# Performance work log

Hardware: AMD Instinct MI355X
Metric: run time of the kernel (lower is better)

The kernel has to match this reference:

```python
import jax, jax.numpy as jnp
import numpy as np

B, L, D_MODEL, H, D_QKV = 4, 2048, 1024, 16, 64
SCALE = float(D_MODEL) ** 0.5  # note: source scales by sqrt(d_model), not sqrt(d_qkv)


def setup_inputs() -> dict:
    key = jax.random.key(0)
    ks = jax.random.split(key, 6)
    xavier_qkv = (2.0 / (D_MODEL + D_QKV)) ** 0.5
    xavier_fc = (2.0 / (H * D_QKV + D_MODEL)) ** 0.5
    return {
        "x": jax.random.normal(ks[0], (B, L, D_MODEL), dtype=jnp.float32),
        "mask": jnp.ones((B, L), dtype=jnp.int32),
        "w_q": jax.random.normal(ks[1], (H, D_MODEL, D_QKV), dtype=jnp.float32) * xavier_qkv,
        "w_k": jax.random.normal(ks[2], (H, D_MODEL, D_QKV), dtype=jnp.float32) * xavier_qkv,
        "w_v": jax.random.normal(ks[3], (H, D_MODEL, D_QKV), dtype=jnp.float32) * xavier_qkv,
        "fc_w": jax.random.normal(ks[4], (D_MODEL, H * D_QKV), dtype=jnp.float32) * xavier_fc,
        "fc_b": jnp.zeros((D_MODEL,), dtype=jnp.float32),
    }


def reference(x, mask, w_q, w_k, w_v, fc_w, fc_b):
    # x: [B, L, M]; per-head projections via einsum, as in the source
    q = jnp.einsum('blm,hmd->blhd', x, w_q)
    k = jnp.einsum('blm,hmd->blhd', x, w_k)
    v = jnp.einsum('blm,hmd->blhd', x, w_v)
    scores = jnp.einsum('blhd,bkhd->bhlk', q, k)  # [B, H, L, L]
    m = mask[:, None, None, :]  # unsqueeze(1).unsqueeze(2)
    scores = jnp.where(m == 0, jnp.asarray(-1e9, scores.dtype), scores)
    logits = jax.nn.softmax(scores / SCALE, axis=3)
    # Faithful to source einsum 'bhlk,blhd->blhd' (k is summed out of logits only)
    out = jnp.einsum('bhlk,blhd->blhd', logits, v)
    out = out.reshape(x.shape[0], x.shape[1], H * D_QKV)
    return out @ fc_w.T + fc_b
```

## Files before the change

kernel.cpp:

```cpp
#include <hip/hip_runtime.h>
#include <hip/hip_bf16.h>


typedef __attribute__((ext_vector_type(8))) short bf16x8;
typedef __attribute__((ext_vector_type(4))) float f32x4;

__device__ __forceinline__ f32x4 mfma16(bf16x8 a, bf16x8 b, f32x4 c) {
  return __builtin_amdgcn_mfma_f32_16x16x32_bf16(a, b, c, 0, 0, 0);
}

__device__ __forceinline__ unsigned short f2b(float f) {
  unsigned int u = __builtin_bit_cast(unsigned int, f);
  return (unsigned short)((u + 0x7fffu + ((u >> 16) & 1u)) >> 16);
}

__device__ __forceinline__ bf16x8 cvt8(float4 a, float4 b) {
  bf16x8 r;
  r[0] = (short)f2b(a.x); r[1] = (short)f2b(a.y); r[2] = (short)f2b(a.z); r[3] = (short)f2b(a.w);
  r[4] = (short)f2b(b.x); r[5] = (short)f2b(b.y); r[6] = (short)f2b(b.z); r[7] = (short)f2b(b.w);
  return r;
}

__device__ __forceinline__ void gld_lds16(const void* g, void* l) {
  __builtin_amdgcn_global_load_lds((const __attribute__((address_space(1))) unsigned int*)g,
                                   (__attribute__((address_space(3))) unsigned int*)l, 16, 0, 0);
}

__global__ __launch_bounds__(256) void prep(const float* __restrict__ x,
                                            const float* __restrict__ wv,
                                            const float* __restrict__ fcw,
                                            unsigned short* __restrict__ xb,
                                            unsigned short* __restrict__ wcT) {
  int bid = blockIdx.x, t = threadIdx.x;
  int wid = t >> 6, lane = t & 63, l16 = lane & 15, quad = lane >> 4;

  if (bid < 256) {
    int wr = wid >> 1, wc = wid & 1;
    int row0 = (bid >> 4) * 64 + wr * 32;
    int col0 = (bid & 15) * 64 + wc * 32;
    f32x4 acc[2][2];
#pragma unroll
    for (int a = 0; a < 2; a++)
#pragma unroll
      for (int b = 0; b < 2; b++) acc[a][b] = (f32x4){0.f, 0.f, 0.f, 0.f};

    float4 A0[2][2], B0[2][2];
#define LOADK(kk, Ad, Bd)                                                            \
    {                                                                                \
      int h_ = (kk) >> 6, d_ = (kk) & 63;                                            \
      _Pragma("unroll")                                                              \
      for (int rt = 0; rt < 2; rt++) {                                               \
        const float* pa = fcw + (row0 + rt * 16 + l16) * 1024 + (kk);                \
        Ad[rt][0] = *reinterpret_cast<const float4*>(pa);                            \
        Ad[rt][1] = *reinterpret_cast<const float4*>(pa + 4);                        \
      }                                                                              \
      _Pragma("unroll")                                                              \
      for (int ct = 0; ct < 2; ct++) {                                               \
        const float* pb = wv + h_ * 65536 + (col0 + ct * 16 + l16) * 64 + d_;        \
        Bd[ct][0] = *reinterpret_cast<const float4*>(pb);                            \
        Bd[ct][1] = *reinterpret_cast<const float4*>(pb + 4);                        \
      }                                                                              \
    }
    LOADK(quad * 8, A0, B0);
    for (int k0 = 0; k0 < 1024; k0 += 32) {
      float4 A1[2][2], B1[2][2];
      if (k0 < 992) LOADK(k0 + 32 + quad * 8, A1, B1);
      bf16x8 af[2], bfr[2];
#pragma unroll
      for (int rt = 0; rt < 2; rt++) af[rt] = cvt8(A0[rt][0], A0[rt][1]);
#pragma unroll
      for (int ct = 0; ct < 2; ct++) bfr[ct] = cvt8(B0[ct][0], B0[ct][1]);
#pragma unroll
      for (int rt = 0; rt < 2; rt++)
#pragma unroll
        for (int ct = 0; ct < 2; ct++) acc[rt][ct] = mfma16(af[rt], bfr[ct], acc[rt][ct]);
#pragma unroll
      for (int a = 0; a < 2; a++)
#pragma unroll
        for (int b = 0; b < 2; b++) { A0[a][b] = A1[a][b]; B0[a][b] = B1[a][b]; }
    }
#undef LOADK
#pragma unroll
    for (int rt = 0; rt < 2; rt++)
#pragma unroll
      for (int ct = 0; ct < 2; ct++) {
        int j0 = row0 + rt * 16 + quad * 4;
        int m = col0 + ct * 16 + l16;
#pragma unroll
        for (int r = 0; r < 4; r++) wcT[(j0 + r) * 1024 + m] = f2b(acc[rt][ct][r]);
      }
  } else {
    int base0 = (bid - 256) << 15;
#pragma unroll
    for (int i = 0; i < 16; i++) {
      int idx = base0 + i * 2048 + t * 8;
      float4 a = *reinterpret_cast<const float4*>(x + idx);
      float4 b = *reinterpret_cast<const float4*>(x + idx + 4);
      *reinterpret_cast<bf16x8*>(xb + idx) = cvt8(a, b);
    }
  }
}

__global__ __launch_bounds__(256, 4) void final_gemm(const unsigned short* __restrict__ xb,
                                                     const unsigned short* __restrict__ wcT,
                                                     const float* __restrict__ fcb,
                                                     float* __restrict__ out) {
  __shared__ __align__(16) unsigned short As[2 * 128 * 32];
  __shared__ __align__(16) unsigned short Bs[2 * 64 * 32];
  int t = threadIdx.x, wid = t >> 6, lane = t & 63, l16 = lane & 15, quad = lane >> 4;
  int wr = wid >> 1, wc = wid & 1;
  int row0 = (blockIdx.x >> 4) * 128;
  int col0 = (blockIdx.x & 15) * 64;

  int w4 = wid * 4, w2 = wid * 2;
  const unsigned short* Ap[4];
  const unsigned short* Bp[2];
#pragma unroll
  for (int j = 0; j < 4; j++) {
    int blk = w4 + j, s = blk >> 3;
    int row = (blk & 7) * 16 + (lane >> 2), kq = lane & 3;
    Ap[j] = xb + (row0 + row) * 1024 + s * 32 + kq * 8;
  }
#pragma unroll
  for (int j = 0; j < 2; j++) {
    int blk = w2 + j, s = blk >> 2;
    int row = (blk & 3) * 16 + (lane >> 2), kq = lane & 3;
    Bp[j] = wcT + (col0 + row) * 1024 + s * 32 + kq * 8;
  }

  f32x4 acc[4][2];
#pragma unroll
  for (int rt = 0; rt < 4; rt++)
#pragma unroll
    for (int ct = 0; ct < 2; ct++) acc[rt][ct] = (f32x4){0.f, 0.f, 0.f, 0.f};

  for (int k0 = 0; k0 < 1024; k0 += 64) {
    __syncthreads();
#pragma unroll
    for (int j = 0; j < 4; j++) gld_lds16(Ap[j] + k0, &As[(w4 + j) * 512 + lane * 8]);
#pragma unroll
    for (int j = 0; j < 2; j++) gld_lds16(Bp[j] + k0, &Bs[(w2 + j) * 512 + lane * 8]);
    __syncthreads();
#pragma unroll
    for (int s = 0; s < 2; s++) {
      bf16x8 af[4], bfr[2];
#pragma unroll
      for (int rt = 0; rt < 4; rt++)
        af[rt] = *reinterpret_cast<const bf16x8*>(&As[s * 4096 + (wr * 64 + rt * 16 + l16) * 32 + quad * 8]);
#pragma unroll
      for (int ct = 0; ct < 2; ct++)
        bfr[ct] = *reinterpret_cast<const bf16x8*>(&Bs[s * 2048 + (wc * 32 + ct * 16 + l16) * 32 + quad * 8]);
#pragma unroll
      for (int rt = 0; rt < 4; rt++)
#pragma unroll
        for (int ct = 0; ct < 2; ct++)
          acc[rt][ct] = mfma16(af[rt], bfr[ct], acc[rt][ct]);
    }
  }

#pragma unroll
  for (int ct = 0; ct < 2; ct++) {
    int j = col0 + wc * 32 + ct * 16 + l16;
    float bias = fcb[j];
#pragma unroll
    for (int rt = 0; rt < 4; rt++) {
      int i0 = row0 + wr * 64 + rt * 16 + quad * 4;
      f32x4 a = acc[rt][ct];
#pragma unroll
      for (int r = 0; r < 4; r++) out[(i0 + r) * 1024 + j] = a[r] + bias;
    }
  }
}

extern "C" void kernel_launch(void* const* d_in, const int* in_sizes, int n_in,
                              void* d_out, int out_size, void* d_ws, size_t ws_size,
                              hipStream_t stream) {
  const float* x   = (const float*)d_in[0];
  const float* wv  = (const float*)d_in[4];
  const float* fcw = (const float*)d_in[5];
  const float* fcb = (const float*)d_in[6];
  float* out = (float*)d_out;

  char* ws = (char*)d_ws;
  unsigned short* xb  = (unsigned short*)(ws);
  unsigned short* wcT = (unsigned short*)(ws + 16777216);

  prep<<<512, 256, 0, stream>>>(x, wv, fcw, xb, wcT);
  final_gemm<<<1024, 256, 0, stream>>>(xb, wcT, fcb, out);
}
```

Before: 151.0 us.

## Double-buffer final GEMM LDS loads and split-K the weight-combine prep kernel

The final GEMM now uses two LDS buffers with a 32-wide K step. The next tile's global→LDS loads are issued before the current tile's MFMAs, and only one barrier runs per iteration, so load latency can overlap with compute. The prep kernel doubles its block size to 512 threads and splits the K loop of the fused weight product across two wave groups, adding their partial sums through shared memory. The prep change drops the explicit register prefetch and adds an LDS reduction and a barrier. The final GEMM relies on the barrier to make the asynchronous LDS loads visible.

```diff
diff --git a/kernel.cpp b/kernel.cpp
--- a/kernel.cpp
+++ b/kernel.cpp
@@ -26,16 +26,17 @@
                                    (__attribute__((address_space(3))) unsigned int*)l, 16, 0, 0);
 }
 
-__global__ __launch_bounds__(256) void prep(const float* __restrict__ x,
+__global__ __launch_bounds__(512) void prep(const float* __restrict__ x,
                                             const float* __restrict__ wv,
                                             const float* __restrict__ fcw,
                                             unsigned short* __restrict__ xb,
                                             unsigned short* __restrict__ wcT) {
+  __shared__ f32x4 red[4][64][4];
   int bid = blockIdx.x, t = threadIdx.x;
   int wid = t >> 6, lane = t & 63, l16 = lane & 15, quad = lane >> 4;
 
   if (bid < 256) {
-    int wr = wid >> 1, wc = wid & 1;
+    int wk = wid >> 2, wr = (wid >> 1) & 1, wc = wid & 1;
     int row0 = (bid >> 4) * 64 + wr * 32;
     int col0 = (bid & 15) * 64 + wc * 32;
     f32x4 acc[2][2];
@@ -44,56 +45,51 @@
 #pragma unroll
       for (int b = 0; b < 2; b++) acc[a][b] = (f32x4){0.f, 0.f, 0.f, 0.f};
 
-    float4 A0[2][2], B0[2][2];
-#define LOADK(kk, Ad, Bd)                                                            \
-    {                                                                                \
-      int h_ = (kk) >> 6, d_ = (kk) & 63;                                            \
-      _Pragma("unroll")                                                              \
-      for (int rt = 0; rt < 2; rt++) {                                               \
-        const float* pa = fcw + (row0 + rt * 16 + l16) * 1024 + (kk);                \
-        Ad[rt][0] = *reinterpret_cast<const float4*>(pa);                            \
-        Ad[rt][1] = *reinterpret_cast<const float4*>(pa + 4);                        \
-      }                                                                              \
-      _Pragma("unroll")                                                              \
-      for (int ct = 0; ct < 2; ct++) {                                               \
-        const float* pb = wv + h_ * 65536 + (col0 + ct * 16 + l16) * 64 + d_;        \
-        Bd[ct][0] = *reinterpret_cast<const float4*>(pb);                            \
-        Bd[ct][1] = *reinterpret_cast<const float4*>(pb + 4);                        \
-      }                                                                              \
-    }
-    LOADK(quad * 8, A0, B0);
-    for (int k0 = 0; k0 < 1024; k0 += 32) {
-      float4 A1[2][2], B1[2][2];
-      if (k0 < 992) LOADK(k0 + 32 + quad * 8, A1, B1);
+    for (int k0 = wk * 512; k0 < wk * 512 + 512; k0 += 32) {
+      int kk = k0 + quad * 8;
+      int h = kk >> 6, d = kk & 63;
       bf16x8 af[2], bfr[2];
 #pragma unroll
-      for (int rt = 0; rt < 2; rt++) af[rt] = cvt8(A0[rt][0], A0[rt][1]);
+      for (int rt = 0; rt < 2; rt++) {
+        const float* pa = fcw + (row0 + rt * 16 + l16) * 1024 + kk;
+        af[rt] = cvt8(*reinterpret_cast<const float4*>(pa), *reinterpret_cast<const float4*>(pa + 4));
+      }
 #pragma unroll
-      for (int ct = 0; ct < 2; ct++) bfr[ct] = cvt8(B0[ct][0], B0[ct][1]);
+      for (int ct = 0; ct < 2; ct++) {
+        const float* pb = wv + h * 65536 + (col0 + ct * 16 + l16) * 64 + d;
+        bfr[ct] = cvt8(*reinterpret_cast<const float4*>(pb), *reinterpret_cast<const float4*>(pb + 4));
+      }
 #pragma unroll
       for (int rt = 0; rt < 2; rt++)
 #pragma unroll
         for (int ct = 0; ct < 2; ct++) acc[rt][ct] = mfma16(af[rt], bfr[ct], acc[rt][ct]);
+    }
+
+    if (wk == 1) {
 #pragma unroll
-      for (int a = 0; a < 2; a++)
+      for (int rt = 0; rt < 2; rt++)
 #pragma unroll
-        for (int b = 0; b < 2; b++) { A0[a][b] = A1[a][b]; B0[a][b] = B1[a][b]; }
+        for (int ct = 0; ct < 2; ct++) red[wid & 3][lane][rt * 2 + ct] = acc[rt][ct];
     }
-#undef LOADK
+    __syncthreads();
+    if (wk == 0) {
 #pragma unroll
-    for (int rt = 0; rt < 2; rt++)
+      for (int rt = 0; rt < 2; rt++)
 #pragma unroll
-      for (int ct = 0; ct < 2; ct++) {
-        int j0 = row0 + rt * 16 + quad * 4;
-        int m = col0 + ct * 16 + l16;
+        for (int ct = 0; ct < 2; ct++) {
+          f32x4 s = acc[rt][ct];
+          f32x4 o = red[wid & 3][lane][rt * 2 + ct];
+          int j0 = row0 + rt * 16 + quad * 4;
+          int m = col0 + ct * 16 + l16;
 #pragma unroll
-        for (int r = 0; r < 4; r++) wcT[(j0 + r) * 1024 + m] = f2b(acc[rt][ct][r]);
-      }
+          for (int r = 0; r < 4; r++) wcT[(j0 + r) * 1024 + m] = f2b(s[r] + o[r]);
+        }
+    }
   } else {
     int base0 = (bid - 256) << 15;
 #pragma unroll
-    for (int i = 0; i < 16; i++) {
-      int idx = base0 + i * 2048 + t * 8;
+    for (int i = 0; i < 8; i++) {
+      int idx = base0 + i * 4096 + t * 8;
       float4 a = *reinterpret_cast<const float4*>(x + idx);
       float4 b = *reinterpret_cast<const float4*>(x + idx + 4);
       *reinterpret_cast<bf16x8*>(xb + idx) = cvt8(a, b);
@@ -105,28 +101,20 @@
                                                      const unsigned short* __restrict__ wcT,
                                                      const float* __restrict__ fcb,
                                                      float* __restrict__ out) {
-  __shared__ __align__(16) unsigned short As[2 * 128 * 32];
-  __shared__ __align__(16) unsigned short Bs[2 * 64 * 32];
+  __shared__ __align__(16) unsigned short As[2][128 * 32];
+  __shared__ __align__(16) unsigned short Bs[2][64 * 32];
   int t = threadIdx.x, wid = t >> 6, lane = t & 63, l16 = lane & 15, quad = lane >> 4;
   int wr = wid >> 1, wc = wid & 1;
   int row0 = (blockIdx.x >> 4) * 128;
   int col0 = (blockIdx.x & 15) * 64;
 
-  int w4 = wid * 4, w2 = wid * 2;
-  const unsigned short* Ap[4];
-  const unsigned short* Bp[2];
-#pragma unroll
-  for (int j = 0; j < 4; j++) {
-    int blk = w4 + j, s = blk >> 3;
-    int row = (blk & 7) * 16 + (lane >> 2), kq = lane & 3;
-    Ap[j] = xb + (row0 + row) * 1024 + s * 32 + kq * 8;
-  }
+  const unsigned short* ApG[2];
 #pragma unroll
   for (int j = 0; j < 2; j++) {
-    int blk = w2 + j, s = blk >> 2;
-    int row = (blk & 3) * 16 + (lane >> 2), kq = lane & 3;
-    Bp[j] = wcT + (col0 + row) * 1024 + s * 32 + kq * 8;
+    int blk = wid * 2 + j;
+    ApG[j] = xb + (row0 + blk * 16 + (lane >> 2)) * 1024 + (lane & 3) * 8;
   }
+  const unsigned short* BpG = wcT + (col0 + wid * 16 + (lane >> 2)) * 1024 + (lane & 3) * 8;
 
   f32x4 acc[4][2];
 #pragma unroll
@@ -134,28 +122,32 @@
 #pragma unroll
     for (int ct = 0; ct < 2; ct++) acc[rt][ct] = (f32x4){0.f, 0.f, 0.f, 0.f};
 
-  for (int k0 = 0; k0 < 1024; k0 += 64) {
+#pragma unroll
+  for (int j = 0; j < 2; j++) gld_lds16(ApG[j], &As[0][(wid * 2 + j) * 512 + lane * 8]);
+  gld_lds16(BpG, &Bs[0][wid * 512 + lane * 8]);
+
+  for (int k = 0; k < 32; k++) {
+    int buf = k & 1;
     __syncthreads();
+    if (k < 31) {
+      int k1 = (k + 1) * 32;
 #pragma unroll
-    for (int j = 0; j < 4; j++) gld_lds16(Ap[j] + k0, &As[(w4 + j) * 512 + lane * 8]);
+      for (int j = 0; j < 2; j++)
+        gld_lds16(ApG[j] + k1, &As[buf ^ 1][(wid * 2 + j) * 512 + lane * 8]);
+      gld_lds16(BpG + k1, &Bs[buf ^ 1][wid * 512 + lane * 8]);
+    }
+    bf16x8 af[4], bfr[2];
 #pragma unroll
-    for (int j = 0; j < 2; j++) gld_lds16(Bp[j] + k0, &Bs[(w2 + j) * 512 + lane * 8]);
-    __syncthreads();
+    for (int rt = 0; rt < 4; rt++)
+      af[rt] = *reinterpret_cast<const bf16x8*>(&As[buf][(wr * 64 + rt * 16 + l16) * 32 + quad * 8]);
 #pragma unroll
-    for (int s = 0; s < 2; s++) {
-      bf16x8 af[4], bfr[2];
+    for (int ct = 0; ct < 2; ct++)
+      bfr[ct] = *reinterpret_cast<const bf16x8*>(&Bs[buf][(wc * 32 + ct * 16 + l16) * 32 + quad * 8]);
 #pragma unroll
-      for (int rt = 0; rt < 4; rt++)
-        af[rt] = *reinterpret_cast<const bf16x8*>(&As[s * 4096 + (wr * 64 + rt * 16 + l16) * 32 + quad * 8]);
+    for (int rt = 0; rt < 4; rt++)
 #pragma unroll
       for (int ct = 0; ct < 2; ct++)
-        bfr[ct] = *reinterpret_cast<const bf16x8*>(&Bs[s * 2048 + (wc * 32 + ct * 16 + l16) * 32 + quad * 8]);
-#pragma unroll
-      for (int rt = 0; rt < 4; rt++)
-#pragma unroll
-        for (int ct = 0; ct < 2; ct++)
-          acc[rt][ct] = mfma16(af[rt], bfr[ct], acc[rt][ct]);
-    }
+        acc[rt][ct] = mfma16(af[rt], bfr[ct], acc[rt][ct]);
   }
 
 #pragma unroll
@@ -185,6 +177,6 @@
   unsigned short* xb  = (unsigned short*)(ws);
   unsigned short* wcT = (unsigned short*)(ws + 16777216);
 
-  prep<<<512, 256, 0, stream>>>(x, wv, fcw, xb, wcT);
+  prep<<<512, 512, 0, stream>>>(x, wv, fcw, xb, wcT);
   final_gemm<<<1024, 256, 0, stream>>>(xb, wcT, fcb, out);
 }
```

After: 155.7 us. 3.1% more time.
